# Kernel tuning notes

Measured on AMD Instinct MI355X. Metric: run time of the kernel, lower is better.

Reference implementation:

```python
import jax, jax.numpy as jnp
import numpy as np

N_CELLS = 10   # nr_cells
CELL = 20      # cell_size (w)
R = 1          # read heads
HID = 128      # controller hidden
IN = 10        # dnc input_size
OUT = 10       # output_dim
CLIP = 20.0
IFACE = R * CELL + 3 * CELL + 5 * R + 3  # 88


def _lstm_step(x, h, c, Wih, Whh, b):
    gates = x @ Wih.T + h @ Whh.T + b
    i, f, g, o = jnp.split(gates, 4, axis=-1)
    c = jax.nn.sigmoid(f) * c + jax.nn.sigmoid(i) * jnp.tanh(g)
    h = jax.nn.sigmoid(o) * jnp.tanh(c)
    return h, c


def _content(mem, keys, strengths):
    # mem (b,n,w), keys (b,k,w), strengths (b,k) -> (b,k,n)
    dot = jnp.einsum('bkw,bnw->bkn', keys, mem)
    kn = jnp.linalg.norm(keys, axis=-1, keepdims=True)
    mn = jnp.linalg.norm(mem, axis=-1)[:, None, :]
    return jax.nn.softmax(dot / (kn * mn + 1e-6) * strengths[..., None], axis=-1)


def _allocate(usage):
    u = 1e-6 + (1.0 - 1e-6) * usage
    idx = jnp.argsort(u, axis=-1)                      # ascending usage
    su = jnp.take_along_axis(u, idx, axis=-1)
    excl = jnp.concatenate([jnp.ones_like(su[:, :1]), jnp.cumprod(su, axis=-1)[:, :-1]], axis=-1)
    sa = (1.0 - su) * excl                             # sorted allocation weights
    inv = jnp.argsort(idx, axis=-1)
    return jnp.take_along_axis(sa, inv, axis=-1)


def _dnc_forward(x, W_ih0, W_hh0, b0, W_ih1, W_hh1, b1, W_if, b_if, W_out, b_out):
    B, T, _ = x.shape
    dt = x.dtype
    z = lambda *s: jnp.zeros(s, dt)
    carry0 = (z(B, HID), z(B, HID), z(B, HID), z(B, HID),   # h0,c0,h1,c1
              z(B, N_CELLS, CELL),                          # memory
              z(B, N_CELLS),                                # usage
              z(B, N_CELLS),                                # precedence
              z(B, N_CELLS, N_CELLS),                       # link matrix
              z(B, R, N_CELLS),                             # read weights
              z(B, N_CELLS),                                # write weights
              z(B, R, CELL))                                # read vectors
    eye = jnp.eye(N_CELLS, dtype=dt)

    def step(carry, xt):
        h0, c0, h1, c1, mem, usage, prec, link, rw, ww, rv = carry
        inp = jnp.concatenate([xt, rv.reshape(B, R * CELL)], axis=-1)
        h0, c0 = _lstm_step(inp, h0, c0, W_ih0, W_hh0, b0)
        h1, c1 = _lstm_step(h0, h1, c1, W_ih1, W_hh1, b1)
        ctrl = jnp.clip(h1, -CLIP, CLIP)
        xi = ctrl @ W_if.T + b_if                            # (B, 88)
        rk = jnp.tanh(xi[:, 0:20]).reshape(B, R, CELL)       # read keys
        rs = jax.nn.softplus(xi[:, 20:21])                   # read strengths
        wk = jnp.tanh(xi[:, 21:41]).reshape(B, 1, CELL)      # write key
        ws = jax.nn.softplus(xi[:, 41:42])                   # write strength
        er = jax.nn.sigmoid(xi[:, 42:62])                    # erase vector
        wv = jnp.tanh(xi[:, 62:82])                          # write vector
        fg = jax.nn.sigmoid(xi[:, 82:83])                    # free gates
        ga = jax.nn.sigmoid(xi[:, 83:84])                    # allocation gate
        gw = jax.nn.sigmoid(xi[:, 84:85])                    # write gate
        modes = jax.nn.softmax(xi[:, 85:88].reshape(B, R, 3), axis=-1)
        # --- write ---
        psi = jnp.prod(1.0 - fg[:, :, None] * rw, axis=1)    # retention (b,n)
        usage = (usage + ww - usage * ww) * psi
        alloc = _allocate(usage)
        cw = _content(mem, wk, ws)[:, 0]                     # (b,n)
        ww = gw * (ga * alloc + (1.0 - ga) * cw)
        mem = mem * (1.0 - ww[:, :, None] * er[:, None, :]) + ww[:, :, None] * wv[:, None, :]
        link = (1.0 - ww[:, :, None] - ww[:, None, :]) * link + ww[:, :, None] * prec[:, None, :]
        link = link * (1.0 - eye)
        prec = (1.0 - ww.sum(-1, keepdims=True)) * prec + ww
        # --- read ---
        fwd_w = jnp.einsum('brn,bmn->brm', rw, link)         # L @ w  (forward)
        bwd_w = jnp.einsum('brn,bnm->brm', rw, link)         # L^T @ w (backward)
        cr = _content(mem, rk, rs)
        rw = modes[..., 0:1] * bwd_w + modes[..., 1:2] * cr + modes[..., 2:3] * fwd_w
        rv = jnp.einsum('brn,bnw->brw', rw, mem)
        o = jnp.concatenate([ctrl, rv.reshape(B, R * CELL)], axis=-1)
        y = o @ W_out.T + b_out
        return (h0, c0, h1, c1, mem, usage, prec, link, rw, ww, rv), y

    _, ys = jax.lax.scan(step, carry0, jnp.swapaxes(x, 0, 1))
    return ys[-1]  # output[:, -1, :]


def setup_inputs() -> dict:
    key = jax.random.key(0)
    ks = jax.random.split(key, 8)
    s = 0.08
    B, T = 512, 512
    return {
        'x': jax.random.normal(ks[0], (B, T, IN), jnp.float32),
        'W_ih0': s * jax.random.normal(ks[1], (4 * HID, IN + R * CELL), jnp.float32),
        'W_hh0': s * jax.random.normal(ks[2], (4 * HID, HID), jnp.float32),
        'b0': jnp.zeros((4 * HID,), jnp.float32),
        'W_ih1': s * jax.random.normal(ks[3], (4 * HID, HID), jnp.float32),
        'W_hh1': s * jax.random.normal(ks[4], (4 * HID, HID), jnp.float32),
        'b1': jnp.zeros((4 * HID,), jnp.float32),
        'W_if': s * jax.random.normal(ks[5], (IFACE, HID), jnp.float32),
        'b_if': jnp.zeros((IFACE,), jnp.float32),
        'W_out': s * jax.random.normal(ks[6], (OUT, HID + R * CELL), jnp.float32),
        'b_out': jnp.zeros((OUT,), jnp.float32),
    }


def reference(x, W_ih0, W_hh0, b0, W_ih1, W_hh1, b1, W_if, b_if, W_out, b_out):
    return _dnc_forward(x, W_ih0, W_hh0, b0, W_ih1, W_hh1, b1, W_if, b_if, W_out, b_out)
```

## Files before the change

### kernel.cpp

```cpp
#include <hip/hip_runtime.h>
#include <math.h>

#define NT 512
#define NB 512
#define HID 128
#define NIN 10
#define NC 10
#define CW 20
#define NIF 88
#define NOUT 10
#define GB 2
#define BLK 512

typedef _Float16 h1;
typedef _Float16 h2 __attribute__((ext_vector_type(2)));

__device__ __forceinline__ float rcpf(float x) { return __builtin_amdgcn_rcpf(x); }
__device__ __forceinline__ float sigf(float x) { return rcpf(1.0f + __expf(-x)); }
__device__ __forceinline__ float tanhf_(float x) {
  float xc = fminf(fmaxf(x, -15.f), 15.f);
  float e = __expf(2.f * xc);
  return (e - 1.f) * rcpf(e + 1.f);
}
__device__ __forceinline__ float splus(float x) { return fmaxf(x, 0.0f) + __logf(1.f + __expf(-fabsf(x))); }

__device__ __forceinline__ float dot2(h2 a, h2 b, float c) {
#if __has_builtin(__builtin_amdgcn_fdot2)
  return __builtin_amdgcn_fdot2(a, b, c, false);
#else
  c += (float)a.x * (float)b.x;
  c += (float)a.y * (float)b.y;
  return c;
#endif
}

__device__ __forceinline__ float bq0(float v) { return __builtin_bit_cast(float, __builtin_amdgcn_ds_swizzle(__builtin_bit_cast(int, v), 0x001C)); }
__device__ __forceinline__ float bq1(float v) { return __builtin_bit_cast(float, __builtin_amdgcn_ds_swizzle(__builtin_bit_cast(int, v), 0x003C)); }
__device__ __forceinline__ float bq2(float v) { return __builtin_bit_cast(float, __builtin_amdgcn_ds_swizzle(__builtin_bit_cast(int, v), 0x005C)); }
__device__ __forceinline__ float bq3(float v) { return __builtin_bit_cast(float, __builtin_amdgcn_ds_swizzle(__builtin_bit_cast(int, v), 0x007C)); }

#define LDSFENCE() do { asm volatile("s_waitcnt lgkmcnt(0)" ::: "memory"); \
                        __builtin_amdgcn_sched_barrier(0); } while (0)

#define BC(f) __builtin_bit_cast(h2, f)

#define DOTF4(W, fa, fb)                                   \
  a0 = dot2(BC((W).x), BC((fa).x), a0);                    \
  a1 = dot2(BC((W).x), BC((fb).x), a1);                    \
  a2 = dot2(BC((W).y), BC((fa).y), a2);                    \
  a3 = dot2(BC((W).y), BC((fb).y), a3);                    \
  a0 = dot2(BC((W).z), BC((fa).z), a0);                    \
  a1 = dot2(BC((W).z), BC((fb).z), a1);                    \
  a2 = dot2(BC((W).w), BC((fa).w), a2);                    \
  a3 = dot2(BC((W).w), BC((fb).w), a3);

#define LSTEP(W, i, Pa, Pb) { float4 fa = (Pa)[i], fb = (Pb)[i]; DOTF4(W, fa, fb) }

__device__ __forceinline__ float4 pack8(const float* p) {
  h2 v0, v1, v2, v3;
  v0.x=(h1)p[0]; v0.y=(h1)p[1]; v1.x=(h1)p[2]; v1.y=(h1)p[3];
  v2.x=(h1)p[4]; v2.y=(h1)p[5]; v3.x=(h1)p[6]; v3.y=(h1)p[7];
  float4 r;
  r.x=__builtin_bit_cast(float,v0); r.y=__builtin_bit_cast(float,v1);
  r.z=__builtin_bit_cast(float,v2); r.w=__builtin_bit_cast(float,v3);
  return r;
}

__device__ __host__ __forceinline__ int rowmap(int s) { return (s & 3) * 128 + (s >> 2); }

__global__ __launch_bounds__(256) void dnc_pack_kernel(
    const float* __restrict__ Wih1, const float* __restrict__ Whh1, float4* __restrict__ ws)
{
  int i = blockIdx.x * 256 + threadIdx.x;
  int s = i & 511, c = i >> 9;
  int R = rowmap(s);
  if (c < 16)      ws[i] = pack8(Whh1 + (size_t)R*HID + 8*c);
  else if (c < 18) ws[i] = pack8(Wih1 + (size_t)R*HID + (14 + (c-16))*8);
}

__global__ __launch_bounds__(BLK)
void dnc_quad_kernel(
    const float* __restrict__ x,
    const float* __restrict__ Wih0, const float* __restrict__ Whh0, const float* __restrict__ b0,
    const float* __restrict__ Wih1, const float* __restrict__ Whh1, const float* __restrict__ b1,
    const float* __restrict__ Wif,  const float* __restrict__ bif,
    const float* __restrict__ Wout, const float* __restrict__ bout,
    const float4* __restrict__ wsT,
    float* __restrict__ out)
{
  __shared__ __align__(16) float4 s_wih1T[14][512];
  __shared__ __align__(16) float4 s_wifT[16*89];
  __shared__ __align__(16) float s_fp[NIF][9];
  __shared__ float s_bif[NIF];
  __shared__ __align__(16) h1   s_xbuf[2][GB][16];
  __shared__ __align__(16) h1   s_rvh[GB][24];
  __shared__ __align__(16) h1   s_h0h[GB][HID];
  __shared__ __align__(16) h1   s_h1h[GB][HID];
  __shared__ __align__(16) h1   s_ctrlh[GB][HID];
  __shared__ __align__(16) float s_ctrl[GB][HID];
  __shared__ __align__(16) float s_mem[GB][NC][CW];
  __shared__ float s_rk[GB][CW], s_wk[GB][CW], s_er[GB][CW], s_wv[GB][CW];
  __shared__ float s_mraw[GB][3];
  __shared__ float s_sc[GB][8];
  __shared__ float s_usage[GB][NC], s_u[GB][NC];
  __shared__ float s_prec[GB][NC], s_prec2[GB][NC];
  __shared__ float s_link[GB][NC][NC];
  __shared__ float s_rw[GB][NC], s_ww[GB][NC];
  __shared__ float s_rv[GB][CW];
  __shared__ float s_cw[GB][NC], s_cr[GB][NC], s_fwd[GB][NC], s_bwd[GB][NC];

  const int tid = threadIdx.x;
  const int bg  = blockIdx.x * GB;
  const int R   = rowmap(tid);

  float4 A0,A1,A2,A3,A4;
  float4 B0,B1,B2,B3,B4,B5,B6,B7,B8,B9,B10,B11,B12,B13,B14,B15;
  float b0r, b1r;
  {
    const float* p = Wih0 + (size_t)R * (NIN + CW);
    A0 = pack8(p);
    { h2 v0,z; v0.x=(h1)p[8]; v0.y=(h1)p[9]; z.x=(h1)0.f; z.y=(h1)0.f;
      float4 f; f.x=__builtin_bit_cast(float,v0); f.y=__builtin_bit_cast(float,z);
      f.z=f.y; f.w=f.y; A1=f; }
    A2 = pack8(p+10); A3 = pack8(p+18);
    { h2 v0,v1,z; v0.x=(h1)p[26]; v0.y=(h1)p[27]; v1.x=(h1)p[28]; v1.y=(h1)p[29];
      z.x=(h1)0.f; z.y=(h1)0.f;
      float4 f; f.x=__builtin_bit_cast(float,v0); f.y=__builtin_bit_cast(float,v1);
      f.z=__builtin_bit_cast(float,z); f.w=f.z; A4=f; }
    const float* q0 = Whh0 + (size_t)R*HID;
    B0 =pack8(q0);    B1 =pack8(q0+8);  B2 =pack8(q0+16);  B3 =pack8(q0+24);
    B4 =pack8(q0+32); B5 =pack8(q0+40); B6 =pack8(q0+48);  B7 =pack8(q0+56);
    B8 =pack8(q0+64); B9 =pack8(q0+72); B10=pack8(q0+80);  B11=pack8(q0+88);
    B12=pack8(q0+96); B13=pack8(q0+104);B14=pack8(q0+112); B15=pack8(q0+120);
    b0r = b0[R]; b1r = b1[R];
  }

  for (int idx = tid; idx < 14*512; idx += BLK) {
    int c = idx >> 9, s = idx & 511;
    s_wih1T[c][s] = pack8(Wih1 + (size_t)rowmap(s)*HID + 8*c);
  }
  for (int idx = tid; idx < 16*NIF; idx += BLK) {
    int j = idx / NIF, q = idx - j*NIF;
    s_wifT[j*89 + q] = pack8(Wif + (size_t)q*HID + 8*j);
  }
  if (tid < NIF) s_bif[tid] = bif[tid];

  if (tid < GB*HID) { int b=tid>>7, j=tid&127;
    s_h0h[b][j]=(h1)0.f; s_h1h[b][j]=(h1)0.f; s_ctrlh[b][j]=(h1)0.f; s_ctrl[b][j]=0.f; }
  for (int i = tid; i < GB*NC*CW; i += BLK) { int b=i/(NC*CW), e=i%(NC*CW);
    s_mem[b][e/CW][e%CW]=0.f; }
  for (int i = tid; i < GB*NC*NC; i += BLK) { int b=i/(NC*NC), e=i%(NC*NC);
    s_link[b][e/NC][e%NC]=0.f; }
  if (tid < GB*NC) { int b=tid/NC, n=tid%NC;
    s_usage[b][n]=0.f; s_prec[b][n]=0.f; s_rw[b][n]=0.f; s_ww[b][n]=0.f; }
  if (tid < GB*CW) { int b=tid/CW, c=tid%CW; s_rv[b][c]=0.f; }
  if (tid < GB*24) { int b=tid/24, c=tid%24; s_rvh[b][c]=(h1)0.f; }
  if (tid < 2*GB*16) { int u=tid, d=u>>5, b=(u>>4)&1, i=u&15;
    float v = 0.f;
    if (d == 0 && i < NIN) v = x[((size_t)(bg+b)*NT + 0)*NIN + i];
    s_xbuf[d][b][i] = (h1)v;
  }
  float c0rA = 0.f, c0rB = 0.f, c1rA = 0.f, c1rB = 0.f;
  __syncthreads();

  auto dnc_tail = [&](int b, int lane) {
    #pragma unroll
    for (int q = lane; q < NIF; q += 64) {
      float a = s_bif[q];
      #pragma unroll
      for (int c = 0; c < 4; ++c) a += s_fp[q][2*c+b];
      if      (q < 20)  s_rk[b][q]    = tanhf_(a);
      else if (q == 20) s_sc[b][0]    = splus(a);
      else if (q < 41)  s_wk[b][q-21] = tanhf_(a);
      else if (q == 41) s_sc[b][1]    = splus(a);
      else if (q < 62)  s_er[b][q-42] = sigf(a);
      else if (q < 82)  s_wv[b][q-62] = tanhf_(a);
      else if (q == 82) s_sc[b][2]    = sigf(a);
      else if (q == 83) s_sc[b][3]    = sigf(a);
      else if (q == 84) s_sc[b][4]    = sigf(a);
      else              s_mraw[b][q-85] = a;
    }
    LDSFENCE();

    if (lane < NC) {
      int n = lane;
      float fg = s_sc[b][2];
      float psi = 1.f - fg * s_rw[b][n];
      float u = s_usage[b][n], w = s_ww[b][n];
      u = (u + w - u*w) * psi;
      s_usage[b][n] = u;
      s_u[b][n] = 1e-6f + (1.0f - 1e-6f) * u;
      float dot=0.f, mn=0.f, kn=0.f;
      #pragma unroll
      for (int c = 0; c < CW; ++c) {
        float m = s_mem[b][n][c], k = s_wk[b][c];
        dot += k*m; mn += m*m; kn += k*k;
      }
      s_cw[b][n] = dot * rcpf(sqrtf(kn)*sqrtf(mn) + 1e-6f) * s_sc[b][1];
    } else if (lane == NC) {
      float m0=s_mraw[b][0], m1=s_mraw[b][1], m2=s_mraw[b][2];
      float mm = fmaxf(m0, fmaxf(m1, m2));
      float e0=__expf(m0-mm), e1=__expf(m1-mm), e2=__expf(m2-mm);
      float es = rcpf(e0+e1+e2);
      s_sc[b][5]=e0*es; s_sc[b][6]=e1*es; s_sc[b][7]=e2*es;
    }
    LDSFENCE();

    if (lane < NC) {
      int n = lane;
      float mx = -1e30f;
      #pragma unroll
      for (int m = 0; m < NC; ++m) mx = fmaxf(mx, s_cw[b][m]);
      float sm = 0.f;
      #pragma unroll
      for (int m = 0; m < NC; ++m) sm += __expf(s_cw[b][m]-mx);
      float cwv = __expf(s_cw[b][n]-mx) * rcpf(sm);
      float un = s_u[b][n];
      float excl = 1.f;
      #pragma unroll
      for (int m = 0; m < NC; ++m) {
        float um = s_u[b][m];
        bool before = (um < un) || (um == un && m < n);
        excl *= before ? um : 1.f;
      }
      float alloc = (1.f - un) * excl;
      float ga = s_sc[b][3], gw = s_sc[b][4];
      s_ww[b][n] = gw * (ga*alloc + (1.f-ga)*cwv);
    }
    LDSFENCE();

    #pragma unroll
    for (int e = lane; e < NC*CW; e += 64) {
      int rr = e/CW, c = e%CW;
      float w = s_ww[b][rr];
      s_mem[b][rr][c] = s_mem[b][rr][c] * (1.f - w*s_er[b][c]) + w*s_wv[b][c];
    }
    #pragma unroll
    for (int e = lane; e < NC*NC; e += 64) {
      int i = e/NC, j = e%NC;
      float wi = s_ww[b][i], wj = s_ww[b][j];
      float l = (1.f - wi - wj)*s_link[b][i][j] + wi*s_prec[b][j];
      s_link[b][i][j] = (i==j) ? 0.f : l;
    }
    if (lane < NC) {
      int n = lane;
      float sw2 = 0.f;
      #pragma unroll
      for (int m = 0; m < NC; ++m) sw2 += s_ww[b][m];
      s_prec2[b][n] = (1.f - sw2)*s_prec[b][n] + s_ww[b][n];
    }
    LDSFENCE();

    if (lane < NC) {
      int m = lane;
      s_prec[b][m] = s_prec2[b][m];
      float a = 0.f;
      #pragma unroll
      for (int n = 0; n < NC; ++n) a += s_rw[b][n]*s_link[b][m][n];
      s_fwd[b][m] = a;
    } else if (lane < 2*NC) {
      int m = lane - NC;
      float a = 0.f;
      #pragma unroll
      for (int n = 0; n < NC; ++n) a += s_rw[b][n]*s_link[b][n][m];
      s_bwd[b][m] = a;
    } else if (lane < 3*NC) {
      int n = lane - 2*NC;
      float dot=0.f, mn=0.f, kn=0.f;
      #pragma unroll
      for (int c = 0; c < CW; ++c) {
        float m = s_mem[b][n][c], k = s_rk[b][c];
        dot += k*m; mn += m*m; kn += k*k;
      }
      s_cr[b][n] = dot * rcpf(sqrtf(kn)*sqrtf(mn)+1e-6f) * s_sc[b][0];
    }
    LDSFENCE();

    if (lane < NC) {
      int n = lane;
      float mx = -1e30f;
      #pragma unroll
      for (int m = 0; m < NC; ++m) mx = fmaxf(mx, s_cr[b][m]);
      float sm = 0.f;
      #pragma unroll
      for (int m = 0; m < NC; ++m) sm += __expf(s_cr[b][m]-mx);
      float cr = __expf(s_cr[b][n]-mx)*rcpf(sm);
      s_rw[b][n] = s_sc[b][5]*s_bwd[b][n] + s_sc[b][6]*cr + s_sc[b][7]*s_fwd[b][n];
    }
    LDSFENCE();

    if (lane < CW) {
      int c = lane;
      float a = 0.f;
      #pragma unroll
      for (int n = 0; n < NC; ++n) a += s_rw[b][n]*s_mem[b][n][c];
      s_rv[b][c] = a;
      s_rvh[b][c] = (h1)a;
    }
  };

  for (int t = 0; t < NT; ++t) {
    const int wv = tid >> 6;
    if (wv >= 6) {
      const int lane = tid & 63, b = wv - 6;
      float xv = 0.f;
      if (lane >= 32 && lane < 32+NIN && (t+1) < NT)
        xv = x[((size_t)(bg+b)*NT + (t+1))*NIN + (lane-32)];
      if (t > 0) {
        __builtin_amdgcn_s_setprio(1);
        dnc_tail(b, lane);
        __builtin_amdgcn_s_setprio(0);
      }
      if (lane >= 32 && lane < 32+NIN && (t+1) < NT)
        s_xbuf[(t+1)&1][b][lane-32] = (h1)xv;
    }
    unsigned lnd = 0;
    asm volatile("" : "+v"(lnd));
    const float4* WS = (const float4*)((const char*)wsT + lnd);
    float4 u0 = WS[0*512+tid], u1 = WS[1*512+tid];
    float4 t0 = WS[2*512+tid], t1 = WS[3*512+tid];
    float r0a, r0b, g1a, g1b;
    {
      float a0=b0r, a1=b0r, a2=0.f, a3=0.f;
      const float4* Xa = (const float4*)&s_xbuf[t&1][0][0];
      const float4* Xb = (const float4*)&s_xbuf[t&1][1][0];
      LSTEP(A0,0,Xa,Xb) LSTEP(A1,1,Xa,Xb)
      const float4* Ha = (const float4*)s_h0h[0];
      const float4* Hb = (const float4*)s_h0h[1];
      LSTEP(B0,0,Ha,Hb)   LSTEP(B1,1,Ha,Hb)   LSTEP(B2,2,Ha,Hb)   LSTEP(B3,3,Ha,Hb)
      LSTEP(B4,4,Ha,Hb)   LSTEP(B5,5,Ha,Hb)   LSTEP(B6,6,Ha,Hb)   LSTEP(B7,7,Ha,Hb)
      LSTEP(B8,8,Ha,Hb)   LSTEP(B9,9,Ha,Hb)   LSTEP(B10,10,Ha,Hb) LSTEP(B11,11,Ha,Hb)
      LSTEP(B12,12,Ha,Hb) LSTEP(B13,13,Ha,Hb) LSTEP(B14,14,Ha,Hb) LSTEP(B15,15,Ha,Hb)
      r0a = a0+a2; r0b = a1+a3;
    }
    {
      float a0=0.f, a1=0.f, a2=0.f, a3=0.f;
      const float4* Ga = (const float4*)s_h1h[0];
      const float4* Gb = (const float4*)s_h1h[1];
      LSTEP(u0, 0,Ga,Gb) LSTEP(u1, 1,Ga,Gb)
      u0 = WS[ 4*512+tid]; u1 = WS[ 5*512+tid];
      LSTEP(t0, 2,Ga,Gb) LSTEP(t1, 3,Ga,Gb)
      t0 = WS[ 6*512+tid]; t1 = WS[ 7*512+tid];
      LSTEP(u0, 4,Ga,Gb) LSTEP(u1, 5,Ga,Gb)
      u0 = WS[ 8*512+tid]; u1 = WS[ 9*512+tid];
      LSTEP(t0, 6,Ga,Gb) LSTEP(t1, 7,Ga,Gb)
      t0 = WS[10*512+tid]; t1 = WS[11*512+tid];
      LSTEP(u0, 8,Ga,Gb) LSTEP(u1, 9,Ga,Gb)
      u0 = WS[12*512+tid]; u1 = WS[13*512+tid];
      LSTEP(t0,10,Ga,Gb) LSTEP(t1,11,Ga,Gb)
      t0 = WS[14*512+tid]; t1 = WS[15*512+tid];
      LSTEP(u0,12,Ga,Gb) LSTEP(u1,13,Ga,Gb)
      LSTEP(t0,14,Ga,Gb) LSTEP(t1,15,Ga,Gb)
      g1a = a0+a2; g1b = a1+a3;
    }
    __syncthreads();

    {
      float a0=r0a, a1=r0b, a2=0.f, a3=0.f;
      const float4* Ra = (const float4*)&s_rvh[0][0];
      const float4* Rb = (const float4*)&s_rvh[1][0];
      LSTEP(A2,0,Ra,Rb) LSTEP(A3,1,Ra,Rb) LSTEP(A4,2,Ra,Rb)
      float gA = a0+a2, gB = a1+a3;
      float giA=bq0(gA), gfA=bq1(gA), ggA=bq2(gA), goA=bq3(gA);
      float giB=bq0(gB), gfB=bq1(gB), ggB=bq2(gB), goB=bq3(gB);
      float cA = sigf(gfA)*c0rA + sigf(giA)*tanhf_(ggA);
      float cB = sigf(gfB)*c0rB + sigf(giB)*tanhf_(ggB);
      c0rA = cA; c0rB = cB;
      float hA = sigf(goA)*tanhf_(cA);
      float hB = sigf(goB)*tanhf_(cB);
      if ((tid & 3) == 0) {
        int u = tid >> 2;
        s_h0h[0][u] = (h1)hA; s_h0h[1][u] = (h1)hB;
      }
    }
    __syncthreads();

    {
      float4 v0 = WS[16*512+tid], v1 = WS[17*512+tid];
      float a0 = g1a + b1r, a1 = g1b + b1r, a2=0.f, a3=0.f;
      const float4* Ha = (const float4*)s_h0h[0];
      const float4* Hb = (const float4*)s_h0h[1];
      { float4 w=s_wih1T[ 0][tid]; LSTEP(w, 0,Ha,Hb) }
      { float4 w=s_wih1T[ 1][tid]; LSTEP(w, 1,Ha,Hb) }
      { float4 w=s_wih1T[ 2][tid]; LSTEP(w, 2,Ha,Hb) }
      { float4 w=s_wih1T[ 3][tid]; LSTEP(w, 3,Ha,Hb) }
      { float4 w=s_wih1T[ 4][tid]; LSTEP(w, 4,Ha,Hb) }
      { float4 w=s_wih1T[ 5][tid]; LSTEP(w, 5,Ha,Hb) }
      { float4 w=s_wih1T[ 6][tid]; LSTEP(w, 6,Ha,Hb) }
      { float4 w=s_wih1T[ 7][tid]; LSTEP(w, 7,Ha,Hb) }
      { float4 w=s_wih1T[ 8][tid]; LSTEP(w, 8,Ha,Hb) }
      { float4 w=s_wih1T[ 9][tid]; LSTEP(w, 9,Ha,Hb) }
      { float4 w=s_wih1T[10][tid]; LSTEP(w,10,Ha,Hb) }
      { float4 w=s_wih1T[11][tid]; LSTEP(w,11,Ha,Hb) }
      { float4 w=s_wih1T[12][tid]; LSTEP(w,12,Ha,Hb) }
      { float4 w=s_wih1T[13][tid]; LSTEP(w,13,Ha,Hb) }
      LSTEP(v0,14,Ha,Hb) LSTEP(v1,15,Ha,Hb)
      float gA = a0+a2, gB = a1+a3;
      float giA=bq0(gA), gfA=bq1(gA), ggA=bq2(gA), goA=bq3(gA);
      float giB=bq0(gB), gfB=bq1(gB), ggB=bq2(gB), goB=bq3(gB);
      float cA = sigf(gfA)*c1rA + sigf(giA)*tanhf_(ggA);
      float cB = sigf(gfB)*c1rB + sigf(giB)*tanhf_(ggB);
      c1rA = cA; c1rB = cB;
      float hA = sigf(goA)*tanhf_(cA);
      float hB = sigf(goB)*tanhf_(cB);
      float clA = fminf(fmaxf(hA, -20.f), 20.f);
      float clB = fminf(fmaxf(hB, -20.f), 20.f);
      if ((tid & 3) == 0) {
        int u = tid >> 2;
        s_h1h[0][u] = (h1)hA;  s_h1h[1][u] = (h1)hB;
        s_ctrl[0][u] = clA;    s_ctrl[1][u] = clB;
        s_ctrlh[0][u] = (h1)clA; s_ctrlh[1][u] = (h1)clB;
      }
    }
    __syncthreads();

    if (tid < 4*NIF) {
      int q = tid >> 2, c = tid & 3;
      float a0=0.f, a1=0.f, a2=0.f, a3=0.f;
      const float4* Ca = (const float4*)s_ctrlh[0];
      const float4* Cb = (const float4*)s_ctrlh[1];
      float4 w0 = s_wifT[(4*c+0)*89 + q];
      float4 w1 = s_wifT[(4*c+1)*89 + q];
      float4 w2 = s_wifT[(4*c+2)*89 + q];
      float4 w3 = s_wifT[(4*c+3)*89 + q];
      LSTEP(w0, 4*c+0, Ca, Cb) LSTEP(w1, 4*c+1, Ca, Cb)
      LSTEP(w2, 4*c+2, Ca, Cb) LSTEP(w3, 4*c+3, Ca, Cb)
      s_fp[q][2*c  ] = a0+a2;
      s_fp[q][2*c+1] = a1+a3;
    }
    __syncthreads();
  }

  if ((tid >> 6) >= 6) dnc_tail((tid >> 6) - 6, tid & 63);
  __syncthreads();

  if (tid < GB*NOUT) {
    int b = tid/NOUT, o = tid%NOUT;
    float a = bout[o];
    const float* Wr = Wout + o*(HID+CW);
    #pragma unroll 4
    for (int k = 0; k < HID; ++k) a += Wr[k]*s_ctrl[b][k];
    #pragma unroll
    for (int c = 0; c < CW; ++c) a += Wr[HID+c]*s_rv[b][c];
    out[(size_t)(bg+b)*NOUT + o] = a;
  }
}

extern "C" void kernel_launch(void* const* d_in, const int* in_sizes, int n_in,
                              void* d_out, int out_size, void* d_ws, size_t ws_size,
                              hipStream_t stream) {
  (void)in_sizes; (void)n_in; (void)out_size; (void)ws_size;
  const float* x    = (const float*)d_in[0];
  const float* Wih0 = (const float*)d_in[1];
  const float* Whh0 = (const float*)d_in[2];
  const float* b0   = (const float*)d_in[3];
  const float* Wih1 = (const float*)d_in[4];
  const float* Whh1 = (const float*)d_in[5];
  const float* b1   = (const float*)d_in[6];
  const float* Wif  = (const float*)d_in[7];
  const float* bif  = (const float*)d_in[8];
  const float* Wout = (const float*)d_in[9];
  const float* bout = (const float*)d_in[10];
  float* out = (float*)d_out;
  float4* ws = (float4*)d_ws;

  dnc_pack_kernel<<<dim3(36), dim3(256), 0, stream>>>(Wih1, Whh1, ws);
  dnc_quad_kernel<<<dim3(NB/GB), dim3(BLK), 0, stream>>>(
      x, Wih0, Whh0, b0, Wih1, Whh1, b1, Wif, bif, Wout, bout, ws, out);
}
```

Before: 6.428 ms.

## Process one batch element per block and shrink LDS for two blocks per CU

Changes the recurrent kernel from two batch elements per 512-thread block to one, launching 512 blocks instead of 256. It cuts the LDS-resident Wih1 slice from 14 to 5 chunks and streams the rest from the global workspace, so LDS usage drops and two blocks can share a CU. The per-step DNC tail now runs on a single 64-lane wave instead of two. The trade-off is that every weight read from LDS or global memory is now amortised over one sequence instead of two, and more Wih1 traffic goes through the cache each step.

```diff
diff --git a/kernel.cpp b/kernel.cpp
--- a/kernel.cpp
+++ b/kernel.cpp
@@ -9,7 +9,6 @@
 #define CW 20
 #define NIF 88
 #define NOUT 10
-#define GB 2
 #define BLK 512
 
 typedef _Float16 h1;
@@ -44,17 +43,13 @@
 
 #define BC(f) __builtin_bit_cast(h2, f)
 
-#define DOTF4(W, fa, fb)                                   \
+#define DOTS4(W, fa)                                       \
   a0 = dot2(BC((W).x), BC((fa).x), a0);                    \
-  a1 = dot2(BC((W).x), BC((fb).x), a1);                    \
   a2 = dot2(BC((W).y), BC((fa).y), a2);                    \
-  a3 = dot2(BC((W).y), BC((fb).y), a3);                    \
   a0 = dot2(BC((W).z), BC((fa).z), a0);                    \
-  a1 = dot2(BC((W).z), BC((fb).z), a1);                    \
-  a2 = dot2(BC((W).w), BC((fa).w), a2);                    \
-  a3 = dot2(BC((W).w), BC((fb).w), a3);
-
-#define LSTEP(W, i, Pa, Pb) { float4 fa = (Pa)[i], fb = (Pb)[i]; DOTF4(W, fa, fb) }
+  a2 = dot2(BC((W).w), BC((fa).w), a2);
+
+#define LST(W, i, Pa) { float4 fa = (Pa)[i]; DOTS4(W, fa) }
 
 __device__ __forceinline__ float4 pack8(const float* p) {
   h2 v0, v1, v2, v3;
@@ -75,11 +70,11 @@
   int s = i & 511, c = i >> 9;
   int R = rowmap(s);
   if (c < 16)      ws[i] = pack8(Whh1 + (size_t)R*HID + 8*c);
-  else if (c < 18) ws[i] = pack8(Wih1 + (size_t)R*HID + (14 + (c-16))*8);
+  else if (c < 27) ws[i] = pack8(Wih1 + (size_t)R*HID + 8*(c - 16 + 5));
 }
 
 __global__ __launch_bounds__(BLK)
-void dnc_quad_kernel(
+void dnc_occ2_kernel(
     const float* __restrict__ x,
     const float* __restrict__ Wih0, const float* __restrict__ Whh0, const float* __restrict__ b0,
     const float* __restrict__ Wih1, const float* __restrict__ Whh1, const float* __restrict__ b1,
@@ -88,29 +83,29 @@
     const float4* __restrict__ wsT,
     float* __restrict__ out)
 {
-  __shared__ __align__(16) float4 s_wih1T[14][512];
+  __shared__ __align__(16) float4 s_wih1T[5][512];
   __shared__ __align__(16) float4 s_wifT[16*89];
-  __shared__ __align__(16) float s_fp[NIF][9];
+  __shared__ __align__(16) float s_fp[NIF][5];
   __shared__ float s_bif[NIF];
-  __shared__ __align__(16) h1   s_xbuf[2][GB][16];
-  __shared__ __align__(16) h1   s_rvh[GB][24];
-  __shared__ __align__(16) h1   s_h0h[GB][HID];
-  __shared__ __align__(16) h1   s_h1h[GB][HID];
-  __shared__ __align__(16) h1   s_ctrlh[GB][HID];
-  __shared__ __align__(16) float s_ctrl[GB][HID];
-  __shared__ __align__(16) float s_mem[GB][NC][CW];
-  __shared__ float s_rk[GB][CW], s_wk[GB][CW], s_er[GB][CW], s_wv[GB][CW];
-  __shared__ float s_mraw[GB][3];
-  __shared__ float s_sc[GB][8];
-  __shared__ float s_usage[GB][NC], s_u[GB][NC];
-  __shared__ float s_prec[GB][NC], s_prec2[GB][NC];
-  __shared__ float s_link[GB][NC][NC];
-  __shared__ float s_rw[GB][NC], s_ww[GB][NC];
-  __shared__ float s_rv[GB][CW];
-  __shared__ float s_cw[GB][NC], s_cr[GB][NC], s_fwd[GB][NC], s_bwd[GB][NC];
+  __shared__ __align__(16) h1   s_xbuf[2][16];
+  __shared__ __align__(16) h1   s_rvh[24];
+  __shared__ __align__(16) h1   s_h0h[HID];
+  __shared__ __align__(16) h1   s_h1h[HID];
+  __shared__ __align__(16) h1   s_ctrlh[HID];
+  __shared__ __align__(16) float s_ctrl[HID];
+  __shared__ __align__(16) float s_mem[NC][CW];
+  __shared__ float s_rk[CW], s_wk[CW], s_er[CW], s_wv[CW];
+  __shared__ float s_mraw[3];
+  __shared__ float s_sc[8];
+  __shared__ float s_usage[NC], s_u[NC];
+  __shared__ float s_prec[NC], s_prec2[NC];
+  __shared__ float s_link[NC][NC];
+  __shared__ float s_rw[NC], s_ww[NC];
+  __shared__ float s_rv[CW];
+  __shared__ float s_cw[NC], s_cr[NC], s_fwd[NC], s_bwd[NC];
 
   const int tid = threadIdx.x;
-  const int bg  = blockIdx.x * GB;
+  const int bg  = blockIdx.x;
   const int R   = rowmap(tid);
 
   float4 A0,A1,A2,A3,A4;
@@ -135,7 +130,7 @@
     b0r = b0[R]; b1r = b1[R];
   }
 
-  for (int idx = tid; idx < 14*512; idx += BLK) {
+  for (int idx = tid; idx < 5*512; idx += BLK) {
     int c = idx >> 9, s = idx & 511;
     s_wih1T[c][s] = pack8(Wih1 + (size_t)rowmap(s)*HID + 8*c);
   }
@@ -145,64 +140,59 @@
   }
   if (tid < NIF) s_bif[tid] = bif[tid];
 
-  if (tid < GB*HID) { int b=tid>>7, j=tid&127;
-    s_h0h[b][j]=(h1)0.f; s_h1h[b][j]=(h1)0.f; s_ctrlh[b][j]=(h1)0.f; s_ctrl[b][j]=0.f; }
-  for (int i = tid; i < GB*NC*CW; i += BLK) { int b=i/(NC*CW), e=i%(NC*CW);
-    s_mem[b][e/CW][e%CW]=0.f; }
-  for (int i = tid; i < GB*NC*NC; i += BLK) { int b=i/(NC*NC), e=i%(NC*NC);
-    s_link[b][e/NC][e%NC]=0.f; }
-  if (tid < GB*NC) { int b=tid/NC, n=tid%NC;
-    s_usage[b][n]=0.f; s_prec[b][n]=0.f; s_rw[b][n]=0.f; s_ww[b][n]=0.f; }
-  if (tid < GB*CW) { int b=tid/CW, c=tid%CW; s_rv[b][c]=0.f; }
-  if (tid < GB*24) { int b=tid/24, c=tid%24; s_rvh[b][c]=(h1)0.f; }
-  if (tid < 2*GB*16) { int u=tid, d=u>>5, b=(u>>4)&1, i=u&15;
+  if (tid < HID) { int j=tid;
+    s_h0h[j]=(h1)0.f; s_h1h[j]=(h1)0.f; s_ctrlh[j]=(h1)0.f; s_ctrl[j]=0.f; }
+  if (tid < NC*CW) s_mem[tid/CW][tid%CW]=0.f;
+  if (tid < NC*NC) s_link[tid/NC][tid%NC]=0.f;
+  if (tid < NC) { s_usage[tid]=0.f; s_prec[tid]=0.f; s_rw[tid]=0.f; s_ww[tid]=0.f; }
+  if (tid < CW) s_rv[tid]=0.f;
+  if (tid < 24) s_rvh[tid]=(h1)0.f;
+  if (tid < 32) { int d=tid>>4, i=tid&15;
     float v = 0.f;
-    if (d == 0 && i < NIN) v = x[((size_t)(bg+b)*NT + 0)*NIN + i];
-    s_xbuf[d][b][i] = (h1)v;
-  }
-  float c0rA = 0.f, c0rB = 0.f, c1rA = 0.f, c1rB = 0.f;
+    if (d == 0 && i < NIN) v = x[((size_t)bg*NT + 0)*NIN + i];
+    s_xbuf[d][i] = (h1)v;
+  }
+  float c0r = 0.f, c1r = 0.f;
   __syncthreads();
 
-  auto dnc_tail = [&](int b, int lane) {
+  auto dnc_tail = [&](int lane) {
     #pragma unroll
     for (int q = lane; q < NIF; q += 64) {
-      float a = s_bif[q];
-      #pragma unroll
-      for (int c = 0; c < 4; ++c) a += s_fp[q][2*c+b];
-      if      (q < 20)  s_rk[b][q]    = tanhf_(a);
-      else if (q == 20) s_sc[b][0]    = splus(a);
-      else if (q < 41)  s_wk[b][q-21] = tanhf_(a);
-      else if (q == 41) s_sc[b][1]    = splus(a);
-      else if (q < 62)  s_er[b][q-42] = sigf(a);
-      else if (q < 82)  s_wv[b][q-62] = tanhf_(a);
-      else if (q == 82) s_sc[b][2]    = sigf(a);
-      else if (q == 83) s_sc[b][3]    = sigf(a);
-      else if (q == 84) s_sc[b][4]    = sigf(a);
-      else              s_mraw[b][q-85] = a;
+      float a = s_bif[q] + s_fp[q][0] + s_fp[q][1] + s_fp[q][2] + s_fp[q][3];
+      if      (q < 20)  s_rk[q]    = tanhf_(a);
+      else if (q == 20) s_sc[0]    = splus(a);
+      else if (q < 41)  s_wk[q-21] = tanhf_(a);
+      else if (q == 41) s_sc[1]    = splus(a);
+      else if (q < 62)  s_er[q-42] = sigf(a);
+      else if (q < 82)  s_wv[q-62] = tanhf_(a);
+      else if (q == 82) s_sc[2]    = sigf(a);
+      else if (q == 83) s_sc[3]    = sigf(a);
+      else if (q == 84) s_sc[4]    = sigf(a);
+      else              s_mraw[q-85] = a;
     }
     LDSFENCE();
 
     if (lane < NC) {
       int n = lane;
-      float fg = s_sc[b][2];
-      float psi = 1.f - fg * s_rw[b][n];
-      float u = s_usage[b][n], w = s_ww[b][n];
+      float fg = s_sc[2];
+      float psi = 1.f - fg * s_rw[n];
+      float u = s_usage[n], w = s_ww[n];
       u = (u + w - u*w) * psi;
-      s_usage[b][n] = u;
-      s_u[b][n] = 1e-6f + (1.0f - 1e-6f) * u;
+      s_usage[n] = u;
+      s_u[n] = 1e-6f + (1.0f - 1e-6f) * u;
       float dot=0.f, mn=0.f, kn=0.f;
       #pragma unroll
       for (int c = 0; c < CW; ++c) {
-        float m = s_mem[b][n][c], k = s_wk[b][c];
+        float m = s_mem[n][c], k = s_wk[c];
         dot += k*m; mn += m*m; kn += k*k;
       }
-      s_cw[b][n] = dot * rcpf(sqrtf(kn)*sqrtf(mn) + 1e-6f) * s_sc[b][1];
+      s_cw[n] = dot * rcpf(sqrtf(kn)*sqrtf(mn) + 1e-6f) * s_sc[1];
     } else if (lane == NC) {
-      float m0=s_mraw[b][0], m1=s_mraw[b][1], m2=s_mraw[b][2];
+      float m0=s_mraw[0], m1=s_mraw[1], m2=s_mraw[2];
       float mm = fmaxf(m0, fmaxf(m1, m2));
       float e0=__expf(m0-mm), e1=__expf(m1-mm), e2=__expf(m2-mm);
       float es = rcpf(e0+e1+e2);
-      s_sc[b][5]=e0*es; s_sc[b][6]=e1*es; s_sc[b][7]=e2*es;
+      s_sc[5]=e0*es; s_sc[6]=e1*es; s_sc[7]=e2*es;
     }
     LDSFENCE();
 
@@ -210,69 +200,69 @@
       int n = lane;
       float mx = -1e30f;
       #pragma unroll
-      for (int m = 0; m < NC; ++m) mx = fmaxf(mx, s_cw[b][m]);
+      for (int m = 0; m < NC; ++m) mx = fmaxf(mx, s_cw[m]);
       float sm = 0.f;
       #pragma unroll
-      for (int m = 0; m < NC; ++m) sm += __expf(s_cw[b][m]-mx);
-      float cwv = __expf(s_cw[b][n]-mx) * rcpf(sm);
-      float un = s_u[b][n];
+      for (int m = 0; m < NC; ++m) sm += __expf(s_cw[m]-mx);
+      float cwv = __expf(s_cw[n]-mx) * rcpf(sm);
+      float un = s_u[n];
       float excl = 1.f;
       #pragma unroll
       for (int m = 0; m < NC; ++m) {
-        float um = s_u[b][m];
+        float um = s_u[m];
         bool before = (um < un) || (um == un && m < n);
         excl *= before ? um : 1.f;
       }
       float alloc = (1.f - un) * excl;
-      float ga = s_sc[b][3], gw = s_sc[b][4];
-      s_ww[b][n] = gw * (ga*alloc + (1.f-ga)*cwv);
+      float ga = s_sc[3], gw = s_sc[4];
+      s_ww[n] = gw * (ga*alloc + (1.f-ga)*cwv);
     }
     LDSFENCE();
 
     #pragma unroll
     for (int e = lane; e < NC*CW; e += 64) {
       int rr = e/CW, c = e%CW;
-      float w = s_ww[b][rr];
-      s_mem[b][rr][c] = s_mem[b][rr][c] * (1.f - w*s_er[b][c]) + w*s_wv[b][c];
+      float w = s_ww[rr];
+      s_mem[rr][c] = s_mem[rr][c] * (1.f - w*s_er[c]) + w*s_wv[c];
     }
     #pragma unroll
     for (int e = lane; e < NC*NC; e += 64) {
       int i = e/NC, j = e%NC;
-      float wi = s_ww[b][i], wj = s_ww[b][j];
-      float l = (1.f - wi - wj)*s_link[b][i][j] + wi*s_prec[b][j];
-      s_link[b][i][j] = (i==j) ? 0.f : l;
+      float wi = s_ww[i], wj = s_ww[j];
+      float l = (1.f - wi - wj)*s_link[i][j] + wi*s_prec[j];
+      s_link[i][j] = (i==j) ? 0.f : l;
     }
     if (lane < NC) {
       int n = lane;
       float sw2 = 0.f;
       #pragma unroll
-      for (int m = 0; m < NC; ++m) sw2 += s_ww[b][m];
-      s_prec2[b][n] = (1.f - sw2)*s_prec[b][n] + s_ww[b][n];
+      for (int m = 0; m < NC; ++m) sw2 += s_ww[m];
+      s_prec2[n] = (1.f - sw2)*s_prec[n] + s_ww[n];
     }
     LDSFENCE();
 
     if (lane < NC) {
       int m = lane;
-      s_prec[b][m] = s_prec2[b][m];
+      s_prec[m] = s_prec2[m];
       float a = 0.f;
       #pragma unroll
-      for (int n = 0; n < NC; ++n) a += s_rw[b][n]*s_link[b][m][n];
-      s_fwd[b][m] = a;
+      for (int n = 0; n < NC; ++n) a += s_rw[n]*s_link[m][n];
+      s_fwd[m] = a;
     } else if (lane < 2*NC) {
       int m = lane - NC;
       float a = 0.f;
       #pragma unroll
-      for (int n = 0; n < NC; ++n) a += s_rw[b][n]*s_link[b][n][m];
-      s_bwd[b][m] = a;
+      for (int n = 0; n < NC; ++n) a += s_rw[n]*s_link[n][m];
+      s_bwd[m] = a;
     } else if (lane < 3*NC) {
       int n = lane - 2*NC;
       float dot=0.f, mn=0.f, kn=0.f;
       #pragma unroll
       for (int c = 0; c < CW; ++c) {
-        float m = s_mem[b][n][c], k = s_rk[b][c];
+        float m = s_mem[n][c], k = s_rk[c];
         dot += k*m; mn += m*m; kn += k*k;
       }
-      s_cr[b][n] = dot * rcpf(sqrtf(kn)*sqrtf(mn)+1e-6f) * s_sc[b][0];
+      s_cr[n] = dot * rcpf(sqrtf(kn)*sqrtf(mn)+1e-6f) * s_sc[0];
     }
     LDSFENCE();
 
@@ -280,12 +270,12 @@
       int n = lane;
       float mx = -1e30f;
       #pragma unroll
-      for (int m = 0; m < NC; ++m) mx = fmaxf(mx, s_cr[b][m]);
+      for (int m = 0; m < NC; ++m) mx = fmaxf(mx, s_cr[m]);
       float sm = 0.f;
       #pragma unroll
-      for (int m = 0; m < NC; ++m) sm += __expf(s_cr[b][m]-mx);
-      float cr = __expf(s_cr[b][n]-mx)*rcpf(sm);
-      s_rw[b][n] = s_sc[b][5]*s_bwd[b][n] + s_sc[b][6]*cr + s_sc[b][7]*s_fwd[b][n];
+      for (int m = 0; m < NC; ++m) sm += __expf(s_cr[m]-mx);
+      float cr = __expf(s_cr[n]-mx)*rcpf(sm);
+      s_rw[n] = s_sc[5]*s_bwd[n] + s_sc[6]*cr + s_sc[7]*s_fwd[n];
     }
     LDSFENCE();
 
@@ -293,156 +283,139 @@
       int c = lane;
       float a = 0.f;
       #pragma unroll
-      for (int n = 0; n < NC; ++n) a += s_rw[b][n]*s_mem[b][n][c];
-      s_rv[b][c] = a;
-      s_rvh[b][c] = (h1)a;
+      for (int n = 0; n < NC; ++n) a += s_rw[n]*s_mem[n][c];
+      s_rv[c] = a;
+      s_rvh[c] = (h1)a;
     }
   };
 
   for (int t = 0; t < NT; ++t) {
-    const int wv = tid >> 6;
-    if (wv >= 6) {
-      const int lane = tid & 63, b = wv - 6;
+    if (tid >= 448) {
+      const int lane = tid - 448;
       float xv = 0.f;
       if (lane >= 32 && lane < 32+NIN && (t+1) < NT)
-        xv = x[((size_t)(bg+b)*NT + (t+1))*NIN + (lane-32)];
+        xv = x[((size_t)bg*NT + (t+1))*NIN + (lane-32)];
       if (t > 0) {
         __builtin_amdgcn_s_setprio(1);
-        dnc_tail(b, lane);
+        dnc_tail(lane);
         __builtin_amdgcn_s_setprio(0);
       }
       if (lane >= 32 && lane < 32+NIN && (t+1) < NT)
-        s_xbuf[(t+1)&1][b][lane-32] = (h1)xv;
+        s_xbuf[(t+1)&1][lane-32] = (h1)xv;
     }
     unsigned lnd = 0;
     asm volatile("" : "+v"(lnd));
     const float4* WS = (const float4*)((const char*)wsT + lnd);
     float4 u0 = WS[0*512+tid], u1 = WS[1*512+tid];
-    float4 t0 = WS[2*512+tid], t1 = WS[3*512+tid];
-    float r0a, r0b, g1a, g1b;
+    float4 u2 = WS[2*512+tid], u3 = WS[3*512+tid];
+    float r0a, g1a;
     {
-      float a0=b0r, a1=b0r, a2=0.f, a3=0.f;
-      const float4* Xa = (const float4*)&s_xbuf[t&1][0][0];
-      const float4* Xb = (const float4*)&s_xbuf[t&1][1][0];
-      LSTEP(A0,0,Xa,Xb) LSTEP(A1,1,Xa,Xb)
-      const float4* Ha = (const float4*)s_h0h[0];
-      const float4* Hb = (const float4*)s_h0h[1];
-      LSTEP(B0,0,Ha,Hb)   LSTEP(B1,1,Ha,Hb)   LSTEP(B2,2,Ha,Hb)   LSTEP(B3,3,Ha,Hb)
-      LSTEP(B4,4,Ha,Hb)   LSTEP(B5,5,Ha,Hb)   LSTEP(B6,6,Ha,Hb)   LSTEP(B7,7,Ha,Hb)
-      LSTEP(B8,8,Ha,Hb)   LSTEP(B9,9,Ha,Hb)   LSTEP(B10,10,Ha,Hb) LSTEP(B11,11,Ha,Hb)
-      LSTEP(B12,12,Ha,Hb) LSTEP(B13,13,Ha,Hb) LSTEP(B14,14,Ha,Hb) LSTEP(B15,15,Ha,Hb)
-      r0a = a0+a2; r0b = a1+a3;
+      float a0=b0r, a2=0.f;
+      const float4* Xa = (const float4*)&s_xbuf[t&1][0];
+      LST(A0,0,Xa) LST(A1,1,Xa)
+      const float4* Ha = (const float4*)s_h0h;
+      LST(B0,0,Ha)   LST(B1,1,Ha)   LST(B2,2,Ha)   LST(B3,3,Ha)
+      LST(B4,4,Ha)   LST(B5,5,Ha)   LST(B6,6,Ha)   LST(B7,7,Ha)
+      LST(B8,8,Ha)   LST(B9,9,Ha)   LST(B10,10,Ha) LST(B11,11,Ha)
+      LST(B12,12,Ha) LST(B13,13,Ha) LST(B14,14,Ha) LST(B15,15,Ha)
+      r0a = a0+a2;
     }
     {
-      float a0=0.f, a1=0.f, a2=0.f, a3=0.f;
-      const float4* Ga = (const float4*)s_h1h[0];
-      const float4* Gb = (const float4*)s_h1h[1];
-      LSTEP(u0, 0,Ga,Gb) LSTEP(u1, 1,Ga,Gb)
+      float a0=0.f, a2=0.f;
+      const float4* Ga = (const float4*)s_h1h;
+      LST(u0, 0,Ga) LST(u1, 1,Ga)
       u0 = WS[ 4*512+tid]; u1 = WS[ 5*512+tid];
-      LSTEP(t0, 2,Ga,Gb) LSTEP(t1, 3,Ga,Gb)
-      t0 = WS[ 6*512+tid]; t1 = WS[ 7*512+tid];
-      LSTEP(u0, 4,Ga,Gb) LSTEP(u1, 5,Ga,Gb)
+      LST(u2, 2,Ga) LST(u3, 3,Ga)
+      u2 = WS[ 6*512+tid]; u3 = WS[ 7*512+tid];
+      LST(u0, 4,Ga) LST(u1, 5,Ga)
       u0 = WS[ 8*512+tid]; u1 = WS[ 9*512+tid];
-      LSTEP(t0, 6,Ga,Gb) LSTEP(t1, 7,Ga,Gb)
-      t0 = WS[10*512+tid]; t1 = WS[11*512+tid];
-      LSTEP(u0, 8,Ga,Gb) LSTEP(u1, 9,Ga,Gb)
+      LST(u2, 6,Ga) LST(u3, 7,Ga)
+      u2 = WS[10*512+tid]; u3 = WS[11*512+tid];
+      LST(u0, 8,Ga) LST(u1, 9,Ga)
       u0 = WS[12*512+tid]; u1 = WS[13*512+tid];
-      LSTEP(t0,10,Ga,Gb) LSTEP(t1,11,Ga,Gb)
-      t0 = WS[14*512+tid]; t1 = WS[15*512+tid];
-      LSTEP(u0,12,Ga,Gb) LSTEP(u1,13,Ga,Gb)
-      LSTEP(t0,14,Ga,Gb) LSTEP(t1,15,Ga,Gb)
-      g1a = a0+a2; g1b = a1+a3;
+      LST(u2,10,Ga) LST(u3,11,Ga)
+      u2 = WS[14*512+tid]; u3 = WS[15*512+tid];
+      LST(u0,12,Ga) LST(u1,13,Ga)
+      LST(u2,14,Ga) LST(u3,15,Ga)
+      g1a = a0+a2;
     }
     __syncthreads();
 
     {
-      float a0=r0a, a1=r0b, a2=0.f, a3=0.f;
-      const float4* Ra = (const float4*)&s_rvh[0][0];
-      const float4* Rb = (const float4*)&s_rvh[1][0];
-      LSTEP(A2,0,Ra,Rb) LSTEP(A3,1,Ra,Rb) LSTEP(A4,2,Ra,Rb)
-      float gA = a0+a2, gB = a1+a3;
-      float giA=bq0(gA), gfA=bq1(gA), ggA=bq2(gA), goA=bq3(gA);
-      float giB=bq0(gB), gfB=bq1(gB), ggB=bq2(gB), goB=bq3(gB);
-      float cA = sigf(gfA)*c0rA + sigf(giA)*tanhf_(ggA);
-      float cB = sigf(gfB)*c0rB + sigf(giB)*tanhf_(ggB);
-      c0rA = cA; c0rB = cB;
-      float hA = sigf(goA)*tanhf_(cA);
-      float hB = sigf(goB)*tanhf_(cB);
+      float a0=r0a, a2=0.f;
+      const float4* Ra = (const float4*)&s_rvh[0];
+      LST(A2,0,Ra) LST(A3,1,Ra) LST(A4,2,Ra)
+      float g = a0+a2;
+      float gi=bq0(g), gf=bq1(g), gg=bq2(g), go=bq3(g);
+      float c = sigf(gf)*c0r + sigf(gi)*tanhf_(gg);
+      c0r = c;
+      float h = sigf(go)*tanhf_(c);
+      if ((tid & 3) == 0) s_h0h[tid >> 2] = (h1)h;
+    }
+    __syncthreads();
+
+    {
+      float4 v0 = WS[16*512+tid], v1 = WS[17*512+tid];
+      float4 v2 = WS[18*512+tid], v3 = WS[19*512+tid];
+      float a0 = g1a + b1r, a2=0.f;
+      const float4* Ha = (const float4*)s_h0h;
+      { float4 w=s_wih1T[0][tid]; LST(w,0,Ha) }
+      { float4 w=s_wih1T[1][tid]; LST(w,1,Ha) }
+      { float4 w=s_wih1T[2][tid]; LST(w,2,Ha) }
+      { float4 w=s_wih1T[3][tid]; LST(w,3,Ha) }
+      { float4 w=s_wih1T[4][tid]; LST(w,4,Ha) }
+      LST(v0, 5,Ha) LST(v1, 6,Ha)
+      v0 = WS[20*512+tid]; v1 = WS[21*512+tid];
+      LST(v2, 7,Ha) LST(v3, 8,Ha)
+      v2 = WS[22*512+tid]; v3 = WS[23*512+tid];
+      LST(v0, 9,Ha) LST(v1,10,Ha)
+      v0 = WS[24*512+tid]; v1 = WS[25*512+tid];
+      LST(v2,11,Ha) LST(v3,12,Ha)
+      v2 = WS[26*512+tid];
+      LST(v0,13,Ha) LST(v1,14,Ha)
+      LST(v2,15,Ha)
+      float g = a0+a2;
+      float gi=bq0(g), gf=bq1(g), gg=bq2(g), go=bq3(g);
+      float c = sigf(gf)*c1r + sigf(gi)*tanhf_(gg);
+      c1r = c;
+      float h = sigf(go)*tanhf_(c);
+      float cl = fminf(fmaxf(h, -20.f), 20.f);
       if ((tid & 3) == 0) {
         int u = tid >> 2;
-        s_h0h[0][u] = (h1)hA; s_h0h[1][u] = (h1)hB;
-      }
-    }
-    __syncthreads();
-
-    {
-      float4 v0 = WS[16*512+tid], v1 = WS[17*512+tid];
-      float a0 = g1a + b1r, a1 = g1b + b1r, a2=0.f, a3=0.f;
-      const float4* Ha = (const float4*)s_h0h[0];
-      const float4* Hb = (const float4*)s_h0h[1];
-      { float4 w=s_wih1T[ 0][tid]; LSTEP(w, 0,Ha,Hb) }
-      { float4 w=s_wih1T[ 1][tid]; LSTEP(w, 1,Ha,Hb) }
-      { float4 w=s_wih1T[ 2][tid]; LSTEP(w, 2,Ha,Hb) }
-      { float4 w=s_wih1T[ 3][tid]; LSTEP(w, 3,Ha,Hb) }
-      { float4 w=s_wih1T[ 4][tid]; LSTEP(w, 4,Ha,Hb) }
-      { float4 w=s_wih1T[ 5][tid]; LSTEP(w, 5,Ha,Hb) }
-      { float4 w=s_wih1T[ 6][tid]; LSTEP(w, 6,Ha,Hb) }
-      { float4 w=s_wih1T[ 7][tid]; LSTEP(w, 7,Ha,Hb) }
-      { float4 w=s_wih1T[ 8][tid]; LSTEP(w, 8,Ha,Hb) }
-      { float4 w=s_wih1T[ 9][tid]; LSTEP(w, 9,Ha,Hb) }
-      { float4 w=s_wih1T[10][tid]; LSTEP(w,10,Ha,Hb) }
-      { float4 w=s_wih1T[11][tid]; LSTEP(w,11,Ha,Hb) }
-      { float4 w=s_wih1T[12][tid]; LSTEP(w,12,Ha,Hb) }
-      { float4 w=s_wih1T[13][tid]; LSTEP(w,13,Ha,Hb) }
-      LSTEP(v0,14,Ha,Hb) LSTEP(v1,15,Ha,Hb)
-      float gA = a0+a2, gB = a1+a3;
-      float giA=bq0(gA), gfA=bq1(gA), ggA=bq2(gA), goA=bq3(gA);
-      float giB=bq0(gB), gfB=bq1(gB), ggB=bq2(gB), goB=bq3(gB);
-      float cA = sigf(gfA)*c1rA + sigf(giA)*tanhf_(ggA);
-      float cB = sigf(gfB)*c1rB + sigf(giB)*tanhf_(ggB);
-      c1rA = cA; c1rB = cB;
-      float hA = sigf(goA)*tanhf_(cA);
-      float hB = sigf(goB)*tanhf_(cB);
-      float clA = fminf(fmaxf(hA, -20.f), 20.f);
-      float clB = fminf(fmaxf(hB, -20.f), 20.f);
-      if ((tid & 3) == 0) {
-        int u = tid >> 2;
-        s_h1h[0][u] = (h1)hA;  s_h1h[1][u] = (h1)hB;
-        s_ctrl[0][u] = clA;    s_ctrl[1][u] = clB;
-        s_ctrlh[0][u] = (h1)clA; s_ctrlh[1][u] = (h1)clB;
+        s_h1h[u] = (h1)h;
+        s_ctrl[u] = cl;
+        s_ctrlh[u] = (h1)cl;
       }
     }
     __syncthreads();
 
     if (tid < 4*NIF) {
       int q = tid >> 2, c = tid & 3;
-      float a0=0.f, a1=0.f, a2=0.f, a3=0.f;
-      const float4* Ca = (const float4*)s_ctrlh[0];
-      const float4* Cb = (const float4*)s_ctrlh[1];
+      float a0=0.f, a2=0.f;
+      const float4* Ca = (const float4*)s_ctrlh;
       float4 w0 = s_wifT[(4*c+0)*89 + q];
       float4 w1 = s_wifT[(4*c+1)*89 + q];
       float4 w2 = s_wifT[(4*c+2)*89 + q];
       float4 w3 = s_wifT[(4*c+3)*89 + q];
-      LSTEP(w0, 4*c+0, Ca, Cb) LSTEP(w1, 4*c+1, Ca, Cb)
-      LSTEP(w2, 4*c+2, Ca, Cb) LSTEP(w3, 4*c+3, Ca, Cb)
-      s_fp[q][2*c  ] = a0+a2;
-      s_fp[q][2*c+1] = a1+a3;
+      LST(w0, 4*c+0, Ca) LST(w1, 4*c+1, Ca)
+      LST(w2, 4*c+2, Ca) LST(w3, 4*c+3, Ca)
+      s_fp[q][c] = a0+a2;
     }
     __syncthreads();
   }
 
-  if ((tid >> 6) >= 6) dnc_tail((tid >> 6) - 6, tid & 63);
+  if (tid >= 448) dnc_tail(tid - 448);
   __syncthreads();
 
-  if (tid < GB*NOUT) {
-    int b = tid/NOUT, o = tid%NOUT;
+  if (tid < NOUT) {
+    int o = tid;
     float a = bout[o];
     const float* Wr = Wout + o*(HID+CW);
     #pragma unroll 4
-    for (int k = 0; k < HID; ++k) a += Wr[k]*s_ctrl[b][k];
+    for (int k = 0; k < HID; ++k) a += Wr[k]*s_ctrl[k];
     #pragma unroll
-    for (int c = 0; c < CW; ++c) a += Wr[HID+c]*s_rv[b][c];
-    out[(size_t)(bg+b)*NOUT + o] = a;
+    for (int c = 0; c < CW; ++c) a += Wr[HID+c]*s_rv[c];
+    out[(size_t)bg*NOUT + o] = a;
   }
 }
 
@@ -464,7 +437,7 @@
   float* out = (float*)d_out;
   float4* ws = (float4*)d_ws;
 
-  dnc_pack_kernel<<<dim3(36), dim3(256), 0, stream>>>(Wih1, Whh1, ws);
-  dnc_quad_kernel<<<dim3(NB/GB), dim3(BLK), 0, stream>>>(
+  dnc_pack_kernel<<<dim3(54), dim3(256), 0, stream>>>(Wih1, Whh1, ws);
+  dnc_occ2_kernel<<<dim3(NB), dim3(BLK), 0, stream>>>(
       x, Wih0, Whh0, b0, Wih1, Whh1, b1, Wif, bif, Wout, bout, ws, out);
 }
```

Result: no change. 6.308 ms (-1.9%).
